# Kernel tuning notes

Hardware: AMD Instinct MI355X
Metric: run time of the kernel (lower is better)

## Reference

```python
import jax, jax.numpy as jnp
import numpy as np

P_FACTOR = 3.0   # config['p_factor']
EPS = 1e-12      # torch F.normalize eps

def _l2_normalize(x):
    return x / jnp.maximum(jnp.linalg.norm(x, axis=-1, keepdims=True), EPS)

def _l1_normalize(x):
    return x / jnp.maximum(jnp.sum(jnp.abs(x), axis=-1, keepdims=True), EPS)

def setup_inputs() -> dict:
    key = jax.random.key(0)
    k = jax.random.split(key, 6)
    B, N_EX, D_IN, D_FEAT, N_LAB, D_CLS = 4096, 16384, 1024, 256, 28, 64
    features = jax.random.normal(k[0], (B, D_IN), jnp.float32)
    labels = jax.random.uniform(k[1], (B, N_LAB), jnp.float32)            # BCE targets in [0,1]
    ex_features = jax.random.normal(k[2], (N_EX, D_IN), jnp.float32)
    ex_classes = jax.random.uniform(k[3], (N_EX, N_LAB), jnp.float32)     # class memberships
    g_w = jax.random.normal(k[4], (D_FEAT, D_IN), jnp.float32) * 0.02     # Linear(in=1024,out=256,bias=False)
    class_reps = jax.random.uniform(k[5], (N_LAB, D_CLS), jnp.float32) * 2.0 - 1.0  # rand*2-1
    return {"features": features, "labels": labels, "ex_features": ex_features,
            "ex_classes": ex_classes, "g_w": g_w, "class_reps": class_reps}

def reference(features, labels, ex_features, ex_classes, g_w, class_reps):
    # g projection (use_g=True, no bias)
    f = features @ g_w.T          # [B, D_FEAT]
    ef = ex_features @ g_w.T      # [N_EX, D_FEAT]
    # exemplar class representations: L1-normalized memberships @ class_reps
    ex_class_reps = _l1_normalize(ex_classes) @ class_reps   # [N_EX, D_CLS]
    # cosine similarity between queries and exemplars
    s = _l2_normalize(f) @ _l2_normalize(ef).T               # [B, N_EX]
    # power-sign activation then L1 normalize over exemplars
    a = _l1_normalize(jnp.sign(s) * jnp.abs(s) ** P_FACTOR)  # [B, N_EX]
    # weighted exemplar aggregation
    echo = a @ ex_class_reps                                  # [B, D_CLS]
    # negative euclidean distances to class representations (cdist)
    diff = echo[:, None, :] - class_reps[None, :, :]          # [B, N_LAB, D_CLS]
    neg_dists = -jnp.sqrt(jnp.sum(diff * diff, axis=-1))      # [B, N_LAB]
    # BCEWithLogitsLoss (mean reduction)
    loss = jnp.mean(-(labels * jax.nn.log_sigmoid(neg_dists)
                      + (1.0 - labels) * jax.nn.log_sigmoid(-neg_dists)))
    return (loss, neg_dists)
```

## Files before the change

kernel.cpp:

```cpp
#include <hip/hip_runtime.h>


typedef __bf16 bf16x8 __attribute__((ext_vector_type(8)));
typedef __bf16 bf16x4 __attribute__((ext_vector_type(4)));
typedef float  f32x4  __attribute__((ext_vector_type(4)));

__device__ __forceinline__ f32x4 f4zero() { f32x4 z = {0.f, 0.f, 0.f, 0.f}; return z; }

__device__ __forceinline__ f32x4 mfma16(bf16x8 a, bf16x8 b, f32x4 c) {
  return __builtin_amdgcn_mfma_f32_16x16x32_bf16(a, b, c, 0, 0, 0);
}

__device__ __forceinline__ bf16x8 load8f(const float* p) {
  f32x4 a = *(const f32x4*)p;
  f32x4 b = *(const f32x4*)(p + 4);
  bf16x8 r;
  r[0] = (__bf16)a[0]; r[1] = (__bf16)a[1]; r[2] = (__bf16)a[2]; r[3] = (__bf16)a[3];
  r[4] = (__bf16)b[0]; r[5] = (__bf16)b[1]; r[6] = (__bf16)b[2]; r[7] = (__bf16)b[3];
  return r;
}

__global__ void zero_f32(float* __restrict__ p, int n) {
  for (int i = blockIdx.x * 256 + threadIdx.x; i < n; i += gridDim.x * 256) p[i] = 0.f;
}

__global__ void fill_sentinel(float* __restrict__ out, int n) {
  for (int i = blockIdx.x * 256 + threadIdx.x; i < n; i += gridDim.x * 256) out[i] = -1.0f;
}

__global__ __launch_bounds__(256, 3)
void proj_l2norm(const float* __restrict__ Xa, const float* __restrict__ Xb,
                 const float* __restrict__ W,
                 __bf16* __restrict__ Pa, __bf16* __restrict__ Pb) {
  __shared__ __align__(16) __bf16 Xs[32 * 72];
  __shared__ __align__(16) __bf16 Ws[256 * 72];
  __shared__ float nrmW[4 * 32];
  __shared__ float invn[32];

  const int tid = threadIdx.x;
  const int w = tid >> 6, lane = tid & 63;
  const int quad = lane >> 4, l15 = lane & 15;

  const float* X;
  __bf16* P;
  int row0;
  if (blockIdx.x < 512) { X = Xa; P = Pa; row0 = blockIdx.x * 32; }
  else                  { X = Xb; P = Pb; row0 = (blockIdx.x - 512) * 32; }

  f32x4 acc[2][4];
#pragma unroll
  for (int i = 0; i < 2; i++)
#pragma unroll
    for (int j = 0; j < 4; j++) acc[i][j] = f4zero();

  for (int ks = 0; ks < 16; ks++) {
    __syncthreads();
    {
      int row = tid >> 3, c8 = tid & 7;
      *(bf16x8*)(Xs + row * 72 + c8 * 8) =
          load8f(X + (size_t)(row0 + row) * 1024 + ks * 64 + c8 * 8);
    }
#pragma unroll
    for (int rep = 0; rep < 8; rep++) {
      int idx = rep * 256 + tid;
      int row = idx >> 3, c8 = idx & 7;
      *(bf16x8*)(Ws + row * 72 + c8 * 8) =
          load8f(W + (size_t)row * 1024 + ks * 64 + c8 * 8);
    }
    __syncthreads();
#pragma unroll
    for (int ksub = 0; ksub < 2; ksub++) {
      bf16x8 af[2], bfr[4];
#pragma unroll
      for (int mb = 0; mb < 2; mb++)
        af[mb] = *(bf16x8*)(Xs + (mb * 16 + l15) * 72 + ksub * 32 + quad * 8);
#pragma unroll
      for (int nb = 0; nb < 4; nb++)
        bfr[nb] = *(bf16x8*)(Ws + (w * 64 + nb * 16 + l15) * 72 + ksub * 32 + quad * 8);
#pragma unroll
      for (int mb = 0; mb < 2; mb++)
#pragma unroll
        for (int nb = 0; nb < 4; nb++)
          acc[mb][nb] = mfma16(af[mb], bfr[nb], acc[mb][nb]);
    }
  }

  float part[2][4];
#pragma unroll
  for (int mb = 0; mb < 2; mb++)
#pragma unroll
    for (int r = 0; r < 4; r++) {
      float s = 0.f;
#pragma unroll
      for (int nb = 0; nb < 4; nb++) { float v = acc[mb][nb][r]; s += v * v; }
      part[mb][r] = s;
    }
#pragma unroll
  for (int m = 1; m < 16; m <<= 1)
#pragma unroll
    for (int mb = 0; mb < 2; mb++)
#pragma unroll
      for (int r = 0; r < 4; r++) part[mb][r] += __shfl_xor(part[mb][r], m, 64);

  if (l15 == 0) {
#pragma unroll
    for (int mb = 0; mb < 2; mb++)
#pragma unroll
      for (int r = 0; r < 4; r++)
        nrmW[w * 32 + mb * 16 + quad * 4 + r] = part[mb][r];
  }
  __syncthreads();
  if (tid < 32) {
    float s = nrmW[tid] + nrmW[32 + tid] + nrmW[64 + tid] + nrmW[96 + tid];
    invn[tid] = 1.0f / fmaxf(sqrtf(s), 1e-12f);
  }
  __syncthreads();
#pragma unroll
  for (int mb = 0; mb < 2; mb++)
#pragma unroll
    for (int nb = 0; nb < 4; nb++)
#pragma unroll
      for (int r = 0; r < 4; r++) {
        int row = mb * 16 + quad * 4 + r;
        int col = w * 64 + nb * 16 + l15;
        P[(size_t)(row0 + row) * 256 + col] = (__bf16)(acc[mb][nb][r] * invn[row]);
      }
}

__global__ void build_vt(const float* __restrict__ exc, __bf16* __restrict__ vT) {
  int e = blockIdx.x * 256 + threadIdx.x;
  float m[28];
  float s = 0.f;
#pragma unroll
  for (int j = 0; j < 28; j++) {
    m[j] = exc[(size_t)e * 28 + j];
    s += fabsf(m[j]);
  }
  float inv = 1.0f / fmaxf(s, 1e-12f);
#pragma unroll
  for (int j = 0; j < 28; j++) vT[(size_t)j * 16384 + e] = (__bf16)(m[j] * inv);
#pragma unroll
  for (int j = 28; j < 32; j++) vT[(size_t)j * 16384 + e] = (__bf16)0.0f;
}

__global__ __launch_bounds__(256, 2)
void fused_sim(const __bf16* __restrict__ fn, const __bf16* __restrict__ efn,
               const __bf16* __restrict__ vTg,
               float* __restrict__ tT, float* __restrict__ r_acc) {
  __shared__ __align__(16) __bf16 Ks[64 * 264];
  __shared__ __align__(16) __bf16 Vs[32 * 72];
  __shared__ __align__(16) __bf16 Us[128 * 72];

  const int tid = threadIdx.x, w = tid >> 6, lane = tid & 63;
  const int quad = lane >> 4, l15 = lane & 15;
  const int wy = w >> 1, wx = w & 1;
  const int chunk = blockIdx.x & 15, mtile = blockIdx.x >> 4;
  const int q0 = mtile * 128;
  const int e_base = chunk * 1024;

  bf16x8 qf[8][4];
#pragma unroll
  for (int ks = 0; ks < 8; ks++)
#pragma unroll
    for (int nb = 0; nb < 4; nb++)
      qf[ks][nb] = *(const bf16x8*)(fn + (size_t)(q0 + wx * 64 + nb * 16 + l15) * 256 +
                                    ks * 32 + quad * 8);

  float r_part[4] = {0.f, 0.f, 0.f, 0.f};
  f32x4 accp[2][2];
#pragma unroll
  for (int a = 0; a < 2; a++)
#pragma unroll
    for (int b = 0; b < 2; b++) accp[a][b] = f4zero();

  for (int t = 0; t < 16; t++) {
    const int e_t = e_base + t * 64;

    __syncthreads();
#pragma unroll
    for (int rep = 0; rep < 8; rep++) {
      int idx = rep * 256 + tid;
      int row = idx >> 5, c8 = idx & 31;
      *(bf16x8*)(Ks + row * 264 + c8 * 8) =
          *(const bf16x8*)(efn + (size_t)(e_t + row) * 256 + c8 * 8);
    }
    {
      int row = tid >> 3, c8 = tid & 7;
      *(bf16x8*)(Vs + row * 72 + c8 * 8) =
          *(const bf16x8*)(vTg + (size_t)row * 16384 + e_t + c8 * 8);
    }
    __syncthreads();

    f32x4 accs[2][4];
#pragma unroll
    for (int a = 0; a < 2; a++)
#pragma unroll
      for (int b = 0; b < 4; b++) accs[a][b] = f4zero();
#pragma unroll
    for (int ks = 0; ks < 8; ks++) {
      bf16x8 af[2];
#pragma unroll
      for (int mb = 0; mb < 2; mb++)
        af[mb] = *(bf16x8*)(Ks + (wy * 32 + mb * 16 + l15) * 264 + ks * 32 + quad * 8);
#pragma unroll
      for (int mb = 0; mb < 2; mb++)
#pragma unroll
        for (int nb = 0; nb < 4; nb++)
          accs[mb][nb] = mfma16(af[mb], qf[ks][nb], accs[mb][nb]);
    }

#pragma unroll
    for (int mb = 0; mb < 2; mb++) {
      const int eo = wy * 32 + mb * 16 + quad * 4;
#pragma unroll
      for (int nb = 0; nb < 4; nb++) {
        const int q = wx * 64 + nb * 16 + l15;
        bf16x4 pk;
#pragma unroll
        for (int r = 0; r < 4; r++) {
          float s = accs[mb][nb][r];
          __bf16 ub = (__bf16)(s * s * s);
          pk[r] = ub;
          r_part[nb] += fabsf((float)ub);
        }
        *(bf16x4*)(Us + q * 72 + eo) = pk;
      }
    }
    __syncthreads();

#pragma unroll
    for (int ks = 0; ks < 2; ks++) {
      bf16x8 vf[2], uf[2];
#pragma unroll
      for (int cb = 0; cb < 2; cb++)
        vf[cb] = *(bf16x8*)(Vs + (cb * 16 + l15) * 72 + ks * 32 + quad * 8);
#pragma unroll
      for (int qb = 0; qb < 2; qb++)
        uf[qb] = *(bf16x8*)(Us + (w * 32 + qb * 16 + l15) * 72 + ks * 32 + quad * 8);
#pragma unroll
      for (int cb = 0; cb < 2; cb++)
#pragma unroll
        for (int qb = 0; qb < 2; qb++)
          accp[cb][qb] = mfma16(vf[cb], uf[qb], accp[cb][qb]);
    }
  }

#pragma unroll
  for (int nb = 0; nb < 4; nb++) {
    float v = r_part[nb];
    v += __shfl_xor(v, 16, 64);
    v += __shfl_xor(v, 32, 64);
    if (quad == 0) atomicAdd(&r_acc[q0 + wx * 64 + nb * 16 + l15], v);
  }
#pragma unroll
  for (int cb = 0; cb < 2; cb++)
#pragma unroll
    for (int qb = 0; qb < 2; qb++)
#pragma unroll
      for (int r = 0; r < 4; r++)
        atomicAdd(&tT[(size_t)(cb * 16 + quad * 4 + r) * 4096 + q0 + w * 32 + qb * 16 + l15],
                  accp[cb][qb][r]);
}

__global__ __launch_bounds__(256, 4)
void finalize(const float* __restrict__ tT, const float* __restrict__ r_acc,
              const float* __restrict__ creps, const float* __restrict__ labels,
              float* __restrict__ loss_acc, float* __restrict__ out) {
  __shared__ __align__(16) float cr[28 * 64];
  __shared__ float wsum[4];
  const int tid = threadIdx.x, w = tid >> 6, lane = tid & 63;
  for (int i = tid; i < 28 * 64; i += 256) cr[i] = creps[i];
  __syncthreads();

  const int q = blockIdx.x * 4 + w;
  float tval = 0.f;
  if (lane < 28) tval = tT[(size_t)lane * 4096 + q];
  tval *= 1.0f / fmaxf(r_acc[q], 1e-12f);

  float echo = 0.f;
#pragma unroll
  for (int j = 0; j < 28; j++)
    echo = fmaf(__shfl(tval, j, 64), cr[j * 64 + lane], echo);

  float dj = 0.f;
#pragma unroll
  for (int j = 0; j < 28; j++) {
    float df = echo - cr[j * 64 + lane];
    float d2 = df * df;
#pragma unroll
    for (int m = 1; m < 64; m <<= 1) d2 += __shfl_xor(d2, m, 64);
    if (lane == j) dj = sqrtf(d2);
  }

  float lsum = 0.f;
  if (lane < 28) {
    out[1 + (size_t)q * 28 + lane] = -dj;
    float y = labels[(size_t)q * 28 + lane];
    lsum = fmaf(y, dj, log1pf(expf(-dj)));
  }
#pragma unroll
  for (int m = 1; m < 64; m <<= 1) lsum += __shfl_xor(lsum, m, 64);
  if (lane == 0) wsum[w] = lsum;
  __syncthreads();
  if (tid == 0) atomicAdd(loss_acc, wsum[0] + wsum[1] + wsum[2] + wsum[3]);
}

__global__ void write_loss(const float* __restrict__ loss_acc, float* __restrict__ out) {
  out[0] = loss_acc[0] * (1.0f / 114688.0f);
}

extern "C" void kernel_launch(void* const* d_in, const int* in_sizes, int n_in,
                              void* d_out, int out_size, void* d_ws, size_t ws_size,
                              hipStream_t stream) {
  const float* features = nullptr;
  const float* labels   = nullptr;
  const float* ex_feat  = nullptr;
  const float* ex_cls   = nullptr;
  const float* g_w      = nullptr;
  const float* creps    = nullptr;
  for (int i = 0; i < n_in; i++) {
    switch (in_sizes[i]) {
      case 4194304:  features = (const float*)d_in[i]; break;
      case 114688:   labels   = (const float*)d_in[i]; break;
      case 16777216: ex_feat  = (const float*)d_in[i]; break;
      case 458752:   ex_cls   = (const float*)d_in[i]; break;
      case 262144:   g_w      = (const float*)d_in[i]; break;
      case 1792:     creps    = (const float*)d_in[i]; break;
      default: break;
    }
  }
  float* out = (float*)d_out;

  if (!features || !labels || !ex_feat || !ex_cls || !g_w || !creps ||
      ws_size < (16ull << 20)) {
    fill_sentinel<<<256, 256, 0, stream>>>(out, out_size);
    return;
  }

  char* ws = (char*)d_ws;
  __bf16* f_n   = (__bf16*)(ws);
  __bf16* ef_n  = (__bf16*)(ws + (2ull << 20));
  __bf16* vT    = (__bf16*)(ws + (10ull << 20));
  float*  tT    = (float*) (ws + (11ull << 20));
  float*  r_acc = tT + 32 * 4096;
  float*  lossp = r_acc + 4096;

  zero_f32<<<528, 256, 0, stream>>>(tT, 32 * 4096 + 4096 + 1);

  proj_l2norm<<<640, 256, 0, stream>>>(ex_feat, features, g_w, ef_n, f_n);
  build_vt<<<64, 256, 0, stream>>>(ex_cls, vT);
  fused_sim<<<512, 256, 0, stream>>>(f_n, ef_n, vT, tT, r_acc);
  finalize<<<1024, 256, 0, stream>>>(tT, r_acc, creps, labels, lossp, out);
  write_loss<<<1, 1, 0, stream>>>(lossp, out);
}
```

Baseline: 253.8 us.

## Pre-convert projection weights to bf16 and stage tiles via direct global-to-LDS loads

Adds a kernel that converts g_w to bf16 once per call in a pre-swizzled tile layout. Both the projection and fused similarity kernels now fill their shared-memory tiles with global_load_lds 16-byte async copies and use an XOR swizzle instead of row padding. This is meant to cut the repeated fp32 weight reads and conversions in every projection block, and to reduce register round-trips and LDS bank conflicts when staging the exemplar tiles. It adds one extra launch plus workspace space, and depends on the builtin's lane-to-LDS address mapping being correct.

Measured after the change: 224.3 us. 11.6% less time.

```diff
diff --git a/kernel.cpp b/kernel.cpp
--- a/kernel.cpp
+++ b/kernel.cpp
@@ -20,6 +20,12 @@
   return r;
 }
 
+__device__ __forceinline__ void async16(const void* g, void* l) {
+  __builtin_amdgcn_global_load_lds(
+      (const __attribute__((address_space(1))) unsigned int*)g,
+      (__attribute__((address_space(3))) unsigned int*)l, 16, 0, 0);
+}
+
 __global__ void zero_f32(float* __restrict__ p, int n) {
   for (int i = blockIdx.x * 256 + threadIdx.x; i < n; i += gridDim.x * 256) p[i] = 0.f;
 }
@@ -28,18 +34,28 @@
   for (int i = blockIdx.x * 256 + threadIdx.x; i < n; i += gridDim.x * 256) out[i] = -1.0f;
 }
 
+__global__ void convert_w(const float* __restrict__ W, __bf16* __restrict__ W2) {
+  int i = blockIdx.x * 256 + threadIdx.x;
+  int ks  = i >> 11;
+  int idx = i & 2047;
+  int row = idx >> 3;
+  int c4  = (idx & 7) ^ (row & 7);
+  *(bf16x8*)(W2 + (size_t)i * 8) = load8f(W + (size_t)row * 1024 + ks * 64 + c4 * 8);
+}
+
 __global__ __launch_bounds__(256, 3)
 void proj_l2norm(const float* __restrict__ Xa, const float* __restrict__ Xb,
-                 const float* __restrict__ W,
+                 const __bf16* __restrict__ W2,
                  __bf16* __restrict__ Pa, __bf16* __restrict__ Pb) {
   __shared__ __align__(16) __bf16 Xs[32 * 72];
-  __shared__ __align__(16) __bf16 Ws[256 * 72];
+  __shared__ __align__(16) __bf16 Ws[256 * 64];
   __shared__ float nrmW[4 * 32];
   __shared__ float invn[32];
 
   const int tid = threadIdx.x;
   const int w = tid >> 6, lane = tid & 63;
   const int quad = lane >> 4, l15 = lane & 15;
+  const int sw = l15 & 7;
 
   const float* X;
   __bf16* P;
@@ -60,12 +76,13 @@
       *(bf16x8*)(Xs + row * 72 + c8 * 8) =
           load8f(X + (size_t)(row0 + row) * 1024 + ks * 64 + c8 * 8);
     }
-#pragma unroll
-    for (int rep = 0; rep < 8; rep++) {
-      int idx = rep * 256 + tid;
-      int row = idx >> 3, c8 = idx & 7;
-      *(bf16x8*)(Ws + row * 72 + c8 * 8) =
-          load8f(W + (size_t)row * 1024 + ks * 64 + c8 * 8);
+    {
+      const __bf16* w2k = W2 + (size_t)ks * 16384;
+#pragma unroll
+      for (int rep = 0; rep < 8; rep++) {
+        int idx = rep * 256 + tid;
+        async16(w2k + idx * 8, Ws + idx * 8);
+      }
     }
     __syncthreads();
 #pragma unroll
@@ -75,8 +92,10 @@
       for (int mb = 0; mb < 2; mb++)
         af[mb] = *(bf16x8*)(Xs + (mb * 16 + l15) * 72 + ksub * 32 + quad * 8);
 #pragma unroll
-      for (int nb = 0; nb < 4; nb++)
-        bfr[nb] = *(bf16x8*)(Ws + (w * 64 + nb * 16 + l15) * 72 + ksub * 32 + quad * 8);
+      for (int nb = 0; nb < 4; nb++) {
+        int c4 = ksub * 4 + quad;
+        bfr[nb] = *(bf16x8*)(Ws + (w * 64 + nb * 16 + l15) * 64 + (c4 ^ sw) * 8);
+      }
 #pragma unroll
       for (int mb = 0; mb < 2; mb++)
 #pragma unroll
@@ -147,17 +166,27 @@
 void fused_sim(const __bf16* __restrict__ fn, const __bf16* __restrict__ efn,
                const __bf16* __restrict__ vTg,
                float* __restrict__ tT, float* __restrict__ r_acc) {
-  __shared__ __align__(16) __bf16 Ks[64 * 264];
+  __shared__ __align__(16) __bf16 Ks[64 * 256];
   __shared__ __align__(16) __bf16 Vs[32 * 72];
   __shared__ __align__(16) __bf16 Us[128 * 72];
 
   const int tid = threadIdx.x, w = tid >> 6, lane = tid & 63;
   const int quad = lane >> 4, l15 = lane & 15;
   const int wy = w >> 1, wx = w & 1;
+  const int swk = l15 & 7;
   const int chunk = blockIdx.x & 15, mtile = blockIdx.x >> 4;
   const int q0 = mtile * 128;
   const int e_base = chunk * 1024;
 
+  int koff[8];
+#pragma unroll
+  for (int rep = 0; rep < 8; rep++) {
+    int idx = rep * 256 + tid;
+    int row = idx >> 5;
+    int c5  = (idx & 31) ^ (row & 7);
+    koff[rep] = row * 256 + c5 * 8;
+  }
+
   bf16x8 qf[8][4];
 #pragma unroll
   for (int ks = 0; ks < 8; ks++)
@@ -177,12 +206,11 @@
     const int e_t = e_base + t * 64;
 
     __syncthreads();
-#pragma unroll
-    for (int rep = 0; rep < 8; rep++) {
-      int idx = rep * 256 + tid;
-      int row = idx >> 5, c8 = idx & 31;
-      *(bf16x8*)(Ks + row * 264 + c8 * 8) =
-          *(const bf16x8*)(efn + (size_t)(e_t + row) * 256 + c8 * 8);
+    {
+      const __bf16* src = efn + (size_t)e_t * 256;
+#pragma unroll
+      for (int rep = 0; rep < 8; rep++)
+        async16(src + koff[rep], Ks + (rep * 256 + tid) * 8);
     }
     {
       int row = tid >> 3, c8 = tid & 7;
@@ -201,7 +229,8 @@
       bf16x8 af[2];
 #pragma unroll
       for (int mb = 0; mb < 2; mb++)
-        af[mb] = *(bf16x8*)(Ks + (wy * 32 + mb * 16 + l15) * 264 + ks * 32 + quad * 8);
+        af[mb] = *(bf16x8*)(Ks + (wy * 32 + mb * 16 + l15) * 256 +
+                            ((ks * 4 + quad) ^ swk) * 8);
 #pragma unroll
       for (int mb = 0; mb < 2; mb++)
 #pragma unroll
@@ -344,10 +373,12 @@
   float*  tT    = (float*) (ws + (11ull << 20));
   float*  r_acc = tT + 32 * 4096;
   float*  lossp = r_acc + 4096;
+  __bf16* W2    = (__bf16*)(ws + (12ull << 20));
 
   zero_f32<<<528, 256, 0, stream>>>(tT, 32 * 4096 + 4096 + 1);
-
-  proj_l2norm<<<640, 256, 0, stream>>>(ex_feat, features, g_w, ef_n, f_n);
+  convert_w<<<128, 256, 0, stream>>>(g_w, W2);
+
+  proj_l2norm<<<640, 256, 0, stream>>>(ex_feat, features, W2, ef_n, f_n);
   build_vt<<<64, 256, 0, stream>>>(ex_cls, vT);
   fused_sim<<<512, 256, 0, stream>>>(f_n, ef_n, vT, tT, r_acc);
   finalize<<<1024, 256, 0, stream>>>(tT, r_acc, creps, labels, lossp, out);
```
